# Optimization experiments

Measured on AMD Instinct MI355X. Metric: run time of the kernel, lower is better.

Reference implementation:

```python
import jax, jax.numpy as jnp
import numpy as np

N_FFT = 2048
STRIDE = 512
PAD = N_FFT // 2  # center padding removed at the end
B = 4
T = 512  # number of spectrogram frames


def _make_kernels():
    n = np.arange(N_FFT)
    # ang[out_sample, freq_bin] = 2*pi*n*k/N  (create_fourier_kernels, freq_scale='no', freq_bins=n_fft)
    ang = 2.0 * np.pi * np.outer(n, n) / N_FFT
    kernel_cos = np.cos(ang).astype(np.float32)
    kernel_sin = np.sin(ang).astype(np.float32)
    # scipy.signal.get_window('hann', N, fftbins=True) -> periodic hann
    window = (0.5 - 0.5 * np.cos(2.0 * np.pi * n / N_FFT)).astype(np.float32)
    return kernel_cos, kernel_sin, window


def setup_inputs() -> dict:
    key = jax.random.key(0)
    X = jax.random.normal(key, (B, N_FFT, T, 2), dtype=jnp.float32)
    kc, ks, w = _make_kernels()
    return {
        "X": X,
        "kernel_cos": jnp.asarray(kc),
        "kernel_sin": jnp.asarray(ks),
        "window": jnp.asarray(w),
    }


def reference(X, kernel_cos, kernel_sin, window):
    # X: (B, n_fft, T, 2) complex spectrogram (onesided=False)
    b, n_fft, t, _ = X.shape
    Xr = X[..., 0]
    Xi = X[..., 1]
    # inverse DFT via dense matmul against sinusoidal kernels (conv2d in torch):
    # frames[b, n, t] = sum_f Xr[b,f,t]*cos(2pi n f/N) - Xi[b,f,t]*sin(2pi n f/N)
    frames = (jnp.einsum('bft,nf->bnt', Xr, kernel_cos)
              - jnp.einsum('bft,nf->bnt', Xi, kernel_sin))
    frames = frames * window[None, :, None] / n_fft
    # overlap-add (torch fold): out[b, t*stride + n] += frames[b, n, t]
    out_len = n_fft + STRIDE * (t - 1)
    idx = (jnp.arange(n_fft)[:, None] + STRIDE * jnp.arange(t)[None, :]).reshape(-1)
    y = jnp.zeros((b, out_len), frames.dtype).at[:, idx].add(frames.reshape(b, -1))
    # window sum-square normalization (torch_window_sumsquare)
    w_sq = jnp.broadcast_to((window * window)[:, None], (n_fft, t)).reshape(-1)
    w_sum = jnp.zeros((out_len,), window.dtype).at[idx].add(w_sq)
    nonzero = w_sum > 1e-10
    denom = jnp.where(nonzero, w_sum, jnp.ones_like(w_sum))
    y = jnp.where(nonzero[None, :], y / denom[None, :], y)
    # center=True, length=None -> trim pad_amount from both ends
    return y[:, PAD:-PAD]
```

## Files before the change

kernel.cpp:

```cpp
#include <hip/hip_runtime.h>

#define NFFT 2048
#define TT   512
#define BB   4
#define OUTL 261632
#define OUTTOT (BB*OUTL)

__device__ __forceinline__ float2 cmul(float2 a, float2 w) {
    return make_float2(a.x * w.x - a.y * w.y, a.x * w.y + a.y * w.x);
}

__device__ __forceinline__ void bf4(const float2 a[4], float2 o[4], float2 w1) {
    float2 w2 = make_float2(w1.x * w1.x - w1.y * w1.y, 2.f * w1.x * w1.y);
    float2 w3 = cmul(w1, w2);
    float t0r = a[0].x + a[2].x, t0i = a[0].y + a[2].y;
    float t1r = a[0].x - a[2].x, t1i = a[0].y - a[2].y;
    float t2r = a[1].x + a[3].x, t2i = a[1].y + a[3].y;
    float t3r = a[3].y - a[1].y, t3i = a[1].x - a[3].x;
    o[0] = make_float2(t0r + t2r, t0i + t2i);
    o[1] = cmul(make_float2(t1r + t3r, t1i + t3i), w1);
    o[2] = cmul(make_float2(t0r - t2r, t0i - t2i), w2);
    o[3] = cmul(make_float2(t1r - t3r, t1i - t3i), w3);
}

template<int SIG> __device__ __forceinline__ int sig(int x) {
    if constexpr (SIG == 0) return x;
    else if constexpr (SIG == 2) return x ^ (((x >> 5) & 3) << 2);
    else                        return x ^ (((x >> 6) & 1) << 4);
}

template<int SBITS, int SR, int SW>
__device__ __forceinline__ void midstage(float* bR, float* bI, int tid,
                                         const float* tw_c, const float* tw_s) {
    const int s = 1 << SBITS;
    float2 ra[4], rb[4];
#pragma unroll
    for (int q = 0; q < 4; q++) {
        int a1 = sig<SR>(tid + 512 * q);
        int a2 = sig<SR>(tid + 256 + 512 * q);
        ra[q] = make_float2(bR[a1], bI[a1]);
        rb[q] = make_float2(bR[a2], bI[a2]);
    }
    __syncthreads();
    const int mA = tid & ~(s - 1), rA = tid & (s - 1);
    const int mB = (tid + 256) & ~(s - 1), rB = (tid + 256) & (s - 1);
    float2 wA = make_float2(tw_c[mA], tw_s[mA]);
    float2 wB = make_float2(tw_c[mB], tw_s[mB]);
    float2 oA[4], oB[4];
    bf4(ra, oA, wA);
    bf4(rb, oB, wB);
    const int jA = 4 * mA + rA, jB = 4 * mB + rB;
#pragma unroll
    for (int k = 0; k < 4; k++) {
        int d1 = sig<SW>(jA + k * s);
        int d2 = sig<SW>(jB + k * s);
        bR[d1] = oA[k].x; bI[d1] = oA[k].y;
        bR[d2] = oB[k].x; bI[d2] = oB[k].y;
    }
    __syncthreads();
}

__global__ __launch_bounds__(256) void fft_k(const float* __restrict__ X,
                                             const float* __restrict__ kc,
                                             const float* __restrict__ ks,
                                             float* __restrict__ Ft) {
    __shared__ float bR[2048];
    __shared__ float bI[2048];
    const int S = blockIdx.x;
    const int c = ((S & 7) << 8) + (((S >> 6) & 31) << 3) + ((S >> 3) & 7);
    const int b = c >> 9;
    const int t = c & 511;
    const int tid = threadIdx.x;
    const float* tw_c = kc + 2048;
    const float* tw_s = ks + 2048;

    const float* Xb = X + ((size_t)(b * 2048) * 512 + t) * 2;
    float2 xa[4], xb_[4];
#pragma unroll
    for (int q = 0; q < 4; q++) {
        xa[q]  = *reinterpret_cast<const float2*>(Xb + (size_t)(tid + 512 * q) * 1024);
        xb_[q] = *reinterpret_cast<const float2*>(Xb + (size_t)(tid + 256 + 512 * q) * 1024);
    }
    float2 w1a = make_float2(tw_c[tid], tw_s[tid]);
    float2 w1b = make_float2(tw_c[tid + 256], tw_s[tid + 256]);
    float2 oA[4], oB[4];
    bf4(xa, oA, w1a);
    bf4(xb_, oB, w1b);
    *reinterpret_cast<float4*>(bR + 4 * tid)         = make_float4(oA[0].x, oA[1].x, oA[2].x, oA[3].x);
    *reinterpret_cast<float4*>(bI + 4 * tid)         = make_float4(oA[0].y, oA[1].y, oA[2].y, oA[3].y);
    *reinterpret_cast<float4*>(bR + 4 * (tid + 256)) = make_float4(oB[0].x, oB[1].x, oB[2].x, oB[3].x);
    *reinterpret_cast<float4*>(bI + 4 * (tid + 256)) = make_float4(oB[0].y, oB[1].y, oB[2].y, oB[3].y);
    __syncthreads();

    midstage<2, 0, 2>(bR, bI, tid, tw_c, tw_s);
    midstage<4, 2, 3>(bR, bI, tid, tw_c, tw_s);
    midstage<6, 3, 0>(bR, bI, tid, tw_c, tw_s);

    float2 aA[4], aB[4];
#pragma unroll
    for (int q = 0; q < 4; q++) {
        aA[q] = make_float2(bR[tid + 512 * q],       bI[tid + 512 * q]);
        aB[q] = make_float2(bR[tid + 256 + 512 * q], bI[tid + 256 + 512 * q]);
    }
    float At0r = aA[0].x + aA[2].x;
    float At1r = aA[0].x - aA[2].x;
    float At2r = aA[1].x + aA[3].x;
    float At3r = aA[3].y - aA[1].y;
    float PA0 = At0r + At2r;
    float PA1 = At1r + At3r;
    float PA2 = At0r - At2r;
    float PA3 = At1r - At3r;
    float Bt0r = aB[0].x + aB[2].x, Bt0i = aB[0].y + aB[2].y;
    float Bt1r = aB[0].x - aB[2].x, Bt1i = aB[0].y - aB[2].y;
    float Bt2r = aB[1].x + aB[3].x, Bt2i = aB[1].y + aB[3].y;
    float Bt3r = aB[3].y - aB[1].y, Bt3i = aB[1].x - aB[3].x;
    const float h = 0.70710678118654752f;
    float PB0 = Bt0r + Bt2r;
    float u1r = Bt1r + Bt3r, u1i = Bt1i + Bt3i;
    float PB1 = h * (u1r - u1i);
    float PB2 = -(Bt0i - Bt2i);
    float u3r = Bt1r - Bt3r, u3i = Bt1i - Bt3i;
    float PB3 = -h * (u3r + u3i);

    float* outp = Ft + (size_t)c * 2048 + tid;
    outp[0]    = PA0 + PB0;
    outp[256]  = PA1 + PB1;
    outp[512]  = PA2 + PB2;
    outp[768]  = PA3 + PB3;
    outp[1024] = PA0 - PB0;
    outp[1280] = PA1 - PB1;
    outp[1536] = PA2 - PB2;
    outp[1792] = PA3 - PB3;
}

__global__ __launch_bounds__(256) void ola_k(const float* __restrict__ Ft,
                                             const float* __restrict__ win,
                                             float* __restrict__ out) {
    int j1 = blockIdx.x * 256 + threadIdx.x;
    if (j1 >= OUTTOT) return;
    int b  = j1 / OUTL;
    int jp = j1 - b * OUTL;
    int j  = jp + 1024;
    int tbase = j >> 9;
    int r = j & 511;
    float acc = 0.f, ws = 0.f;
    #pragma unroll
    for (int k = 0; k < 4; k++) {
        int t = tbase - k;
        if (t >= 0 && t < TT) {
            int n = r + (k << 9);
            float w = win[n];
            acc += Ft[(size_t)(b * TT + t) * NFFT + n] * w;
            ws  += w * w;
        }
    }
    float y = acc * (1.0f / (float)NFFT);
    if (ws > 1e-10f) y /= ws;
    out[j1] = y;
}

extern "C" void kernel_launch(void* const* d_in, const int* in_sizes, int n_in,
                              void* d_out, int out_size, void* d_ws, size_t ws_size,
                              hipStream_t stream) {
    const float* X  = (const float*)d_in[0];
    const float* kc = (const float*)d_in[1];
    const float* ks = (const float*)d_in[2];
    const float* w  = (const float*)d_in[3];
    float* out = (float*)d_out;

    float* Ft = (float*)d_ws;

    fft_k<<<dim3(BB * TT), dim3(256), 0, stream>>>(X, kc, ks, Ft);
    ola_k<<<dim3((OUTTOT + 255) / 256), dim3(256), 0, stream>>>(Ft, w, out);
}
```

Baseline: 34.35 us.

## Fuse FFT and overlap-add into one kernel with redundant halo frames

Merges the per-frame inverse FFT and the overlap-add normalization into a single kernel. Each block computes the seven frames overlapping its 2048-sample output segment, two at a time in shared memory, and accumulates windowed frames in registers. This removes the intermediate frame buffer round-trip through global memory and a second launch. In exchange, it recomputes frames at segment boundaries (about 1.75x FFT work and X reads) and runs fewer, larger blocks in a serial 4-round loop.

```diff
diff --git a/kernel.cpp b/kernel.cpp
--- a/kernel.cpp
+++ b/kernel.cpp
@@ -4,7 +4,6 @@
 #define TT   512
 #define BB   4
 #define OUTL 261632
-#define OUTTOT (BB*OUTL)
 
 __device__ __forceinline__ float2 cmul(float2 a, float2 w) {
     return make_float2(a.x * w.x - a.y * w.y, a.x * w.y + a.y * w.x);
@@ -30,20 +29,20 @@
 }
 
 template<int SBITS, int SR, int SW>
-__device__ __forceinline__ void midstage(float* bR, float* bI, int tid,
+__device__ __forceinline__ void midstage(float* bR, float* bI, int tid2,
                                          const float* tw_c, const float* tw_s) {
     const int s = 1 << SBITS;
     float2 ra[4], rb[4];
 #pragma unroll
     for (int q = 0; q < 4; q++) {
-        int a1 = sig<SR>(tid + 512 * q);
-        int a2 = sig<SR>(tid + 256 + 512 * q);
+        int a1 = sig<SR>(tid2 + 512 * q);
+        int a2 = sig<SR>(tid2 + 256 + 512 * q);
         ra[q] = make_float2(bR[a1], bI[a1]);
         rb[q] = make_float2(bR[a2], bI[a2]);
     }
     __syncthreads();
-    const int mA = tid & ~(s - 1), rA = tid & (s - 1);
-    const int mB = (tid + 256) & ~(s - 1), rB = (tid + 256) & (s - 1);
+    const int mA = tid2 & ~(s - 1), rA = tid2 & (s - 1);
+    const int mB = (tid2 + 256) & ~(s - 1), rB = (tid2 + 256) & (s - 1);
     float2 wA = make_float2(tw_c[mA], tw_s[mA]);
     float2 wB = make_float2(tw_c[mB], tw_s[mB]);
     float2 oA[4], oB[4];
@@ -60,103 +59,133 @@
     __syncthreads();
 }
 
-__global__ __launch_bounds__(256) void fft_k(const float* __restrict__ X,
-                                             const float* __restrict__ kc,
-                                             const float* __restrict__ ks,
-                                             float* __restrict__ Ft) {
-    __shared__ float bR[2048];
-    __shared__ float bI[2048];
+__global__ __launch_bounds__(512) void istft_k(const float* __restrict__ X,
+                                               const float* __restrict__ kc,
+                                               const float* __restrict__ ks,
+                                               const float* __restrict__ win,
+                                               float* __restrict__ out) {
+    __shared__ float bR[2][2048];
+    __shared__ float bI[2][2048];
+    __shared__ float fr[2][2048];
+
     const int S = blockIdx.x;
-    const int c = ((S & 7) << 8) + (((S >> 6) & 31) << 3) + ((S >> 3) & 7);
-    const int b = c >> 9;
-    const int t = c & 511;
-    const int tid = threadIdx.x;
+    const int G = ((S & 7) << 6) + (S >> 3);
+    const int b = G >> 7;
+    const int R = G & 127;
+    const int tidall = threadIdx.x;
+    const int h = tidall >> 8;
+    const int tid2 = tidall & 255;
     const float* tw_c = kc + 2048;
     const float* tw_s = ks + 2048;
-
-    const float* Xb = X + ((size_t)(b * 2048) * 512 + t) * 2;
-    float2 xa[4], xb_[4];
+    float* hbR = bR[h];
+    float* hbI = bI[h];
+
+    float acc[4] = {0.f, 0.f, 0.f, 0.f};
+
+#pragma unroll 1
+    for (int round = 0; round < 4; ++round) {
+        const int m = 2 * round + h;
+        const int t = 4 * R - 1 + m;
+        const bool valid = (t >= 0) && (t < TT) && (m < 7);
+
+        const float* Xb = X + (((size_t)b * 2048) * 512 + (valid ? t : 0)) * 2;
+        float2 xa[4], xb_[4];
+#pragma unroll
+        for (int q = 0; q < 4; q++) {
+            if (valid) {
+                xa[q]  = *reinterpret_cast<const float2*>(Xb + (size_t)(tid2 + 512 * q) * 1024);
+                xb_[q] = *reinterpret_cast<const float2*>(Xb + (size_t)(tid2 + 256 + 512 * q) * 1024);
+            } else {
+                xa[q] = make_float2(0.f, 0.f);
+                xb_[q] = make_float2(0.f, 0.f);
+            }
+        }
+        float2 w1a = make_float2(tw_c[tid2], tw_s[tid2]);
+        float2 w1b = make_float2(tw_c[tid2 + 256], tw_s[tid2 + 256]);
+        float2 oA[4], oB[4];
+        bf4(xa, oA, w1a);
+        bf4(xb_, oB, w1b);
+        *reinterpret_cast<float4*>(hbR + 4 * tid2)         = make_float4(oA[0].x, oA[1].x, oA[2].x, oA[3].x);
+        *reinterpret_cast<float4*>(hbI + 4 * tid2)         = make_float4(oA[0].y, oA[1].y, oA[2].y, oA[3].y);
+        *reinterpret_cast<float4*>(hbR + 4 * (tid2 + 256)) = make_float4(oB[0].x, oB[1].x, oB[2].x, oB[3].x);
+        *reinterpret_cast<float4*>(hbI + 4 * (tid2 + 256)) = make_float4(oB[0].y, oB[1].y, oB[2].y, oB[3].y);
+        __syncthreads();
+
+        midstage<2, 0, 2>(hbR, hbI, tid2, tw_c, tw_s);
+        midstage<4, 2, 3>(hbR, hbI, tid2, tw_c, tw_s);
+        midstage<6, 3, 0>(hbR, hbI, tid2, tw_c, tw_s);
+
+        float2 aA[4], aB[4];
+#pragma unroll
+        for (int q = 0; q < 4; q++) {
+            aA[q] = make_float2(hbR[tid2 + 512 * q],       hbI[tid2 + 512 * q]);
+            aB[q] = make_float2(hbR[tid2 + 256 + 512 * q], hbI[tid2 + 256 + 512 * q]);
+        }
+        float At0r = aA[0].x + aA[2].x;
+        float At1r = aA[0].x - aA[2].x;
+        float At2r = aA[1].x + aA[3].x;
+        float At3r = aA[3].y - aA[1].y;
+        float PA0 = At0r + At2r;
+        float PA1 = At1r + At3r;
+        float PA2 = At0r - At2r;
+        float PA3 = At1r - At3r;
+        float Bt0r = aB[0].x + aB[2].x, Bt0i = aB[0].y + aB[2].y;
+        float Bt1r = aB[0].x - aB[2].x, Bt1i = aB[0].y - aB[2].y;
+        float Bt2r = aB[1].x + aB[3].x, Bt2i = aB[1].y + aB[3].y;
+        float Bt3r = aB[3].y - aB[1].y, Bt3i = aB[1].x - aB[3].x;
+        const float hc = 0.70710678118654752f;
+        float PB0 = Bt0r + Bt2r;
+        float u1r = Bt1r + Bt3r, u1i = Bt1i + Bt3i;
+        float PB1 = hc * (u1r - u1i);
+        float PB2 = -(Bt0i - Bt2i);
+        float u3r = Bt1r - Bt3r, u3i = Bt1i - Bt3i;
+        float PB3 = -hc * (u3r + u3i);
+
+        float* fh = fr[h];
+        fh[tid2]        = (PA0 + PB0) * win[tid2];
+        fh[tid2 + 256]  = (PA1 + PB1) * win[tid2 + 256];
+        fh[tid2 + 512]  = (PA2 + PB2) * win[tid2 + 512];
+        fh[tid2 + 768]  = (PA3 + PB3) * win[tid2 + 768];
+        fh[tid2 + 1024] = (PA0 - PB0) * win[tid2 + 1024];
+        fh[tid2 + 1280] = (PA1 - PB1) * win[tid2 + 1280];
+        fh[tid2 + 1536] = (PA2 - PB2) * win[tid2 + 1536];
+        fh[tid2 + 1792] = (PA3 - PB3) * win[tid2 + 1792];
+        __syncthreads();
+
+#pragma unroll
+        for (int hh = 0; hh < 2; hh++) {
+            int mm = 2 * round + hh;
+            int base = tidall + 1536 - (mm << 9);
+#pragma unroll
+            for (int q = 0; q < 4; q++) {
+                int n = base + (q << 9);
+                if (n >= 0 && n < 2048) acc[q] += fr[hh][n];
+            }
+        }
+        __syncthreads();
+    }
+
 #pragma unroll
     for (int q = 0; q < 4; q++) {
-        xa[q]  = *reinterpret_cast<const float2*>(Xb + (size_t)(tid + 512 * q) * 1024);
-        xb_[q] = *reinterpret_cast<const float2*>(Xb + (size_t)(tid + 256 + 512 * q) * 1024);
-    }
-    float2 w1a = make_float2(tw_c[tid], tw_s[tid]);
-    float2 w1b = make_float2(tw_c[tid + 256], tw_s[tid + 256]);
-    float2 oA[4], oB[4];
-    bf4(xa, oA, w1a);
-    bf4(xb_, oB, w1b);
-    *reinterpret_cast<float4*>(bR + 4 * tid)         = make_float4(oA[0].x, oA[1].x, oA[2].x, oA[3].x);
-    *reinterpret_cast<float4*>(bI + 4 * tid)         = make_float4(oA[0].y, oA[1].y, oA[2].y, oA[3].y);
-    *reinterpret_cast<float4*>(bR + 4 * (tid + 256)) = make_float4(oB[0].x, oB[1].x, oB[2].x, oB[3].x);
-    *reinterpret_cast<float4*>(bI + 4 * (tid + 256)) = make_float4(oB[0].y, oB[1].y, oB[2].y, oB[3].y);
-    __syncthreads();
-
-    midstage<2, 0, 2>(bR, bI, tid, tw_c, tw_s);
-    midstage<4, 2, 3>(bR, bI, tid, tw_c, tw_s);
-    midstage<6, 3, 0>(bR, bI, tid, tw_c, tw_s);
-
-    float2 aA[4], aB[4];
-#pragma unroll
-    for (int q = 0; q < 4; q++) {
-        aA[q] = make_float2(bR[tid + 512 * q],       bI[tid + 512 * q]);
-        aB[q] = make_float2(bR[tid + 256 + 512 * q], bI[tid + 256 + 512 * q]);
-    }
-    float At0r = aA[0].x + aA[2].x;
-    float At1r = aA[0].x - aA[2].x;
-    float At2r = aA[1].x + aA[3].x;
-    float At3r = aA[3].y - aA[1].y;
-    float PA0 = At0r + At2r;
-    float PA1 = At1r + At3r;
-    float PA2 = At0r - At2r;
-    float PA3 = At1r - At3r;
-    float Bt0r = aB[0].x + aB[2].x, Bt0i = aB[0].y + aB[2].y;
-    float Bt1r = aB[0].x - aB[2].x, Bt1i = aB[0].y - aB[2].y;
-    float Bt2r = aB[1].x + aB[3].x, Bt2i = aB[1].y + aB[3].y;
-    float Bt3r = aB[3].y - aB[1].y, Bt3i = aB[1].x - aB[3].x;
-    const float h = 0.70710678118654752f;
-    float PB0 = Bt0r + Bt2r;
-    float u1r = Bt1r + Bt3r, u1i = Bt1i + Bt3i;
-    float PB1 = h * (u1r - u1i);
-    float PB2 = -(Bt0i - Bt2i);
-    float u3r = Bt1r - Bt3r, u3i = Bt1i - Bt3i;
-    float PB3 = -h * (u3r + u3i);
-
-    float* outp = Ft + (size_t)c * 2048 + tid;
-    outp[0]    = PA0 + PB0;
-    outp[256]  = PA1 + PB1;
-    outp[512]  = PA2 + PB2;
-    outp[768]  = PA3 + PB3;
-    outp[1024] = PA0 - PB0;
-    outp[1280] = PA1 - PB1;
-    outp[1536] = PA2 - PB2;
-    outp[1792] = PA3 - PB3;
-}
-
-__global__ __launch_bounds__(256) void ola_k(const float* __restrict__ Ft,
-                                             const float* __restrict__ win,
-                                             float* __restrict__ out) {
-    int j1 = blockIdx.x * 256 + threadIdx.x;
-    if (j1 >= OUTTOT) return;
-    int b  = j1 / OUTL;
-    int jp = j1 - b * OUTL;
-    int j  = jp + 1024;
-    int tbase = j >> 9;
-    int r = j & 511;
-    float acc = 0.f, ws = 0.f;
-    #pragma unroll
-    for (int k = 0; k < 4; k++) {
-        int t = tbase - k;
-        if (t >= 0 && t < TT) {
-            int n = r + (k << 9);
-            float w = win[n];
-            acc += Ft[(size_t)(b * TT + t) * NFFT + n] * w;
-            ws  += w * w;
-        }
-    }
-    float y = acc * (1.0f / (float)NFFT);
-    if (ws > 1e-10f) y /= ws;
-    out[j1] = y;
+        int jl = tidall + (q << 9);
+        int jp = (R << 11) + jl;
+        if (jp < OUTL) {
+            int j = jp + 1024;
+            int tb = j >> 9, r = j & 511;
+            float ws = 0.f;
+#pragma unroll
+            for (int k = 0; k < 4; k++) {
+                int t = tb - k;
+                if (t >= 0 && t < TT) {
+                    float w = win[r + (k << 9)];
+                    ws += w * w;
+                }
+            }
+            float y = acc[q] * (1.0f / 2048.0f);
+            if (ws > 1e-10f) y /= ws;
+            out[(size_t)b * OUTL + jp] = y;
+        }
+    }
 }
 
 extern "C" void kernel_launch(void* const* d_in, const int* in_sizes, int n_in,
@@ -168,8 +197,5 @@
     const float* w  = (const float*)d_in[3];
     float* out = (float*)d_out;
 
-    float* Ft = (float*)d_ws;
-
-    fft_k<<<dim3(BB * TT), dim3(256), 0, stream>>>(X, kc, ks, Ft);
-    ola_k<<<dim3((OUTTOT + 255) / 256), dim3(256), 0, stream>>>(Ft, w, out);
-}
+    istft_k<<<dim3(BB * 128), dim3(512), 0, stream>>>(X, kc, ks, w, out);
+}
```

New measurement: 54.95 us. 60.0% more time.
